# Optimization experiments

Measured on AMD Instinct MI355X. Metric: run time of the kernel, lower is better.

## Reference

```python
import jax, jax.numpy as jnp
import numpy as np

R = 131072          # total proposals (ROIs)
D = 1024            # input feature dim (ShapeSpec.channels)
NUM_CLASSES = 80    # COCO foreground classes
REID_DIM = 256      # reid_feat_dim
BOX_DIM = 4


def setup_inputs() -> dict:
    key = jax.random.key(0)
    ks = jax.random.split(key, 12)
    x = jax.random.normal(ks[0], (R, D), dtype=jnp.float32)
    # cls_score: Linear(D, num_classes+1), init std=0.01, bias 0
    W_cls = 0.01 * jax.random.normal(ks[1], (NUM_CLASSES + 1, D), dtype=jnp.float32)
    b_cls = jnp.zeros((NUM_CLASSES + 1,), dtype=jnp.float32)
    # bbox_pred: Linear(D, num_classes * 4), init std=0.001, bias 0
    W_bbox = 0.001 * jax.random.normal(ks[2], (NUM_CLASSES * BOX_DIM, D), dtype=jnp.float32)
    b_bbox = jnp.zeros((NUM_CLASSES * BOX_DIM,), dtype=jnp.float32)
    # reid_embed_head: MLP(D, 256, 256, 3) -> Linear(D,256), Linear(256,256), Linear(256,256)
    def lin(k, fan_in, fan_out):
        kw, kb = jax.random.split(k)
        bound = 1.0 / np.sqrt(fan_in)
        W = jax.random.uniform(kw, (fan_out, fan_in), minval=-bound, maxval=bound, dtype=jnp.float32)
        b = jax.random.uniform(kb, (fan_out,), minval=-bound, maxval=bound, dtype=jnp.float32)
        return W, b
    W1, b1 = lin(ks[3], D, REID_DIM)
    W2, b2 = lin(ks[4], REID_DIM, REID_DIM)
    W3, b3 = lin(ks[5], REID_DIM, REID_DIM)
    return {"x": x, "W_cls": W_cls, "b_cls": b_cls, "W_bbox": W_bbox, "b_bbox": b_bbox,
            "W1": W1, "b1": b1, "W2": W2, "b2": b2, "W3": W3, "b3": b3}


def reference(x, W_cls, b_cls, W_bbox, b_bbox, W1, b1, W2, b2, W3, b3):
    # x: [R, D] (already flat; torch forward flattens if dim > 2)
    scores = x @ W_cls.T + b_cls                 # [R, K+1]
    proposal_deltas = x @ W_bbox.T + b_bbox      # [R, K*4]
    # MLP with ReLU on all but last layer
    h = jax.nn.relu(x @ W1.T + b1)               # [R, 256]
    h = jax.nn.relu(h @ W2.T + b2)               # [R, 256]
    embeds = h @ W3.T + b3                       # [R, 256]
    return scores, proposal_deltas, embeds
```

## Files before the change

kernel.cpp:

```cpp
#include <hip/hip_runtime.h>
#include <hip/hip_bf16.h>
#include <stdint.h>

#define R_TOT   131072
#define D_IN    1024
#define N_CLS   81
#define N_BOX   320
#define N_H     256
#define N1_USED 657
#define N1_PAD  768
#define NB_COLS 384

typedef __attribute__((ext_vector_type(8))) short short8;
typedef __attribute__((ext_vector_type(4))) float f32x4;

__device__ __forceinline__ unsigned short f2bf(float f) {
  union { float f; unsigned u; } v; v.f = f;
  unsigned r = v.u + 0x7FFFu + ((v.u >> 16) & 1u);
  return (unsigned short)(r >> 16);
}

__device__ __forceinline__ short8 cvt8(float4 a, float4 b) {
  short8 v;
  v[0] = (short)f2bf(a.x); v[1] = (short)f2bf(a.y);
  v[2] = (short)f2bf(a.z); v[3] = (short)f2bf(a.w);
  v[4] = (short)f2bf(b.x); v[5] = (short)f2bf(b.y);
  v[6] = (short)f2bf(b.z); v[7] = (short)f2bf(b.w);
  return v;
}

__device__ __forceinline__ void async_lds16(void* lds, const void* g) {
  __builtin_amdgcn_global_load_lds(
      (const __attribute__((address_space(1))) unsigned int*)g,
      (__attribute__((address_space(3))) unsigned int*)lds, 16, 0, 0);
}

__global__ void prep_w1(const float* __restrict__ Wc, const float* __restrict__ Wb,
                        const float* __restrict__ W1, unsigned short* __restrict__ Wp)
{
  int idx = blockIdx.x * 256 + threadIdx.x;
  int p   = idx / (N1_PAD * 32);
  int rem = idx % (N1_PAD * 32);
  int n   = rem >> 5;
  int kk  = rem & 31;
  int k   = p * 32 + kk;
  float w = 0.f;
  if (n < N_CLS)               w = Wc[(size_t)n * D_IN + k];
  else if (n < N_CLS + N_BOX)  w = Wb[(size_t)(n - N_CLS) * D_IN + k];
  else if (n < N1_USED)        w = W1[(size_t)(n - (N_CLS + N_BOX)) * D_IN + k];
  Wp[idx] = f2bf(w);
}

__global__ void prep_w23(const float* __restrict__ W2, const float* __restrict__ W3,
                         unsigned short* __restrict__ W2b, unsigned short* __restrict__ W3b)
{
  int idx = blockIdx.x * 256 + threadIdx.x;
  if (idx < 65536) W2b[idx] = f2bf(W2[idx]);
  else             W3b[idx - 65536] = f2bf(W3[idx - 65536]);
}

__global__ __launch_bounds__(512) void g1_kernel(
    const float* __restrict__ x, const unsigned short* __restrict__ Wp,
    const float* __restrict__ b_cls, const float* __restrict__ b_box,
    const float* __restrict__ b1,
    float* __restrict__ scores, float* __restrict__ deltas,
    unsigned short* __restrict__ h1)
{
  __shared__ __attribute__((aligned(16))) unsigned short As[64 * 256];

  const int tid  = threadIdx.x;
  const int wave = tid >> 6;
  const int lane = tid & 63;
  const int orig  = blockIdx.x;
  const int work  = (orig & 7) * 512 + (orig >> 3);
  const int m0    = (work >> 1) * 64;
  const int nbase = (work & 1) * NB_COLS;

  const int lr  = lane & 15;
  const int hig = lane >> 4;
  const int g2  = hig * 8;

  f32x4 acc[4][3];
#pragma unroll
  for (int i = 0; i < 4; ++i)
#pragma unroll
    for (int j = 0; j < 3; ++j)
      acc[i][j] = (f32x4){0.f, 0.f, 0.f, 0.f};

  const unsigned short* bptr = Wp + (size_t)(nbase + wave * 48 + lr) * 32 + g2;
  const size_t BSTEP = (size_t)N1_PAD * 32;

  short8 bCur0 = *(const short8*)(bptr);
  short8 bCur1 = *(const short8*)(bptr + 512);
  short8 bCur2 = *(const short8*)(bptr + 1024);
  bptr += BSTEP;

#pragma unroll 2
  for (int kp = 0; kp < 32; ++kp) {
    const int kk = kp & 7;

    if (kk == 0) {
      if (kp > 0) __syncthreads();
      const int c0 = (kp >> 3) * 256;
#pragma unroll
      for (int i = 0; i < 4; ++i) {
        int idx = tid + i * 512;
        int row = idx >> 5, s = idx & 31;
        const float* src = x + (size_t)(m0 + row) * D_IN + c0 + s * 8;
        float4 f0 = *(const float4*)src;
        float4 f1 = *(const float4*)(src + 4);
        *(short8*)&As[row * 256 + ((s ^ (row & 7)) << 3)] = cvt8(f0, f1);
      }
      __syncthreads();
    }

    short8 bn0, bn1, bn2;
    if (kp < 31) {
      bn0 = *(const short8*)(bptr);
      bn1 = *(const short8*)(bptr + 512);
      bn2 = *(const short8*)(bptr + 1024);
      bptr += BSTEP;
    }

    const int sb = kk * 4 + hig;
    __builtin_amdgcn_s_setprio(1);
#pragma unroll
    for (int mi = 0; mi < 4; ++mi) {
      const int r  = mi * 16 + lr;
      const int sl = sb ^ (r & 7);
      short8 af = *(const short8*)&As[r * 256 + (sl << 3)];
      acc[mi][0] = __builtin_amdgcn_mfma_f32_16x16x32_bf16(af, bCur0, acc[mi][0], 0, 0, 0);
      acc[mi][1] = __builtin_amdgcn_mfma_f32_16x16x32_bf16(af, bCur1, acc[mi][1], 0, 0, 0);
      acc[mi][2] = __builtin_amdgcn_mfma_f32_16x16x32_bf16(af, bCur2, acc[mi][2], 0, 0, 0);
    }
    __builtin_amdgcn_s_setprio(0);

    if (kp < 31) { bCur0 = bn0; bCur1 = bn1; bCur2 = bn2; }
  }

  const int rbase = m0 + (hig << 2);
#pragma unroll
  for (int mi = 0; mi < 4; ++mi) {
#pragma unroll
    for (int ni = 0; ni < 3; ++ni) {
      int n = nbase + wave * 48 + ni * 16 + lr;
      if (n >= N1_USED) continue;
      if (n < N_CLS) {
        float bb = b_cls[n];
#pragma unroll
        for (int j = 0; j < 4; ++j) {
          int r = rbase + mi * 16 + j;
          scores[(size_t)r * N_CLS + n] = acc[mi][ni][j] + bb;
        }
      } else if (n < N_CLS + N_BOX) {
        int nb = n - N_CLS;
        float bb = b_box[nb];
#pragma unroll
        for (int j = 0; j < 4; ++j) {
          int r = rbase + mi * 16 + j;
          deltas[(size_t)r * N_BOX + nb] = acc[mi][ni][j] + bb;
        }
      } else {
        int nh = n - (N_CLS + N_BOX);
        float bb = b1[nh];
#pragma unroll
        for (int j = 0; j < 4; ++j) {
          int r = rbase + mi * 16 + j;
          float h = acc[mi][ni][j] + bb;
          h1[(size_t)r * N_H + nh] = f2bf(fmaxf(h, 0.f));
        }
      }
    }
  }
}

__device__ __forceinline__ void g23_stage(unsigned short* Asb, unsigned short* Bsb,
    const unsigned short* __restrict__ A, const unsigned short* __restrict__ Bw,
    int m0, int kp, int tid)
{
  {
    int row = tid >> 2, kq = tid & 3;
    async_lds16((char*)Asb + tid * 16,
                (const char*)(A + (size_t)(m0 + row) * N_H + (size_t)kp * 32 + kq * 8));
  }
#pragma unroll
  for (int i = 0; i < 2; ++i) {
    int chunk = tid + i * 512;
    int row = chunk >> 2, kq = chunk & 3;
    async_lds16((char*)Bsb + chunk * 16,
                (const char*)(Bw + (size_t)row * N_H + (size_t)kp * 32 + kq * 8));
  }
}

template <int RELU, int OUT_BF16>
__global__ __launch_bounds__(512, 1) void g23_kernel(
    const unsigned short* __restrict__ A, const unsigned short* __restrict__ Bw,
    const float* __restrict__ bias, void* __restrict__ outv)
{
  __shared__ __attribute__((aligned(16))) unsigned short As[2][128 * 32];
  __shared__ __attribute__((aligned(16))) unsigned short Bs[2][256 * 32];
  const int tid  = threadIdx.x;
  const int wave = tid >> 6, lane = tid & 63;
  const int wm = wave >> 2, wn = wave & 3;
  const int m0 = blockIdx.x * 128;

  f32x4 acc[4][4];
#pragma unroll
  for (int i = 0; i < 4; ++i)
#pragma unroll
    for (int j = 0; j < 4; ++j)
      acc[i][j] = (f32x4){0.f, 0.f, 0.f, 0.f};

  g23_stage(&As[0][0], &Bs[0][0], A, Bw, m0, 0, tid);
  __syncthreads();

  const int lr = lane & 15;
  const int lk = (lane >> 4) * 8;

  for (int kp = 0; kp < 8; ++kp) {
    const int cur = kp & 1, nxt = cur ^ 1;
    if (kp < 7) g23_stage(&As[nxt][0], &Bs[nxt][0], A, Bw, m0, kp + 1, tid);

    short8 af[4], bfr[4];
#pragma unroll
    for (int mi = 0; mi < 4; ++mi)
      af[mi] = *(const short8*)&As[cur][(wm * 64 + mi * 16 + lr) * 32 + lk];
#pragma unroll
    for (int ni = 0; ni < 4; ++ni)
      bfr[ni] = *(const short8*)&Bs[cur][(wn * 64 + ni * 16 + lr) * 32 + lk];
#pragma unroll
    for (int mi = 0; mi < 4; ++mi)
#pragma unroll
      for (int ni = 0; ni < 4; ++ni)
        acc[mi][ni] = __builtin_amdgcn_mfma_f32_16x16x32_bf16(af[mi], bfr[ni], acc[mi][ni], 0, 0, 0);
    __syncthreads();
  }

#pragma unroll
  for (int mi = 0; mi < 4; ++mi) {
#pragma unroll
    for (int ni = 0; ni < 4; ++ni) {
      int n = wn * 64 + ni * 16 + lr;
      float bb = bias[n];
#pragma unroll
      for (int j = 0; j < 4; ++j) {
        int r = m0 + wm * 64 + mi * 16 + ((lane >> 4) << 2) + j;
        float v = acc[mi][ni][j] + bb;
        if (RELU) v = fmaxf(v, 0.f);
        if (OUT_BF16) ((unsigned short*)outv)[(size_t)r * N_H + n] = f2bf(v);
        else          ((float*)outv)[(size_t)r * N_H + n] = v;
      }
    }
  }
}

extern "C" void kernel_launch(void* const* d_in, const int* in_sizes, int n_in,
                              void* d_out, int out_size, void* d_ws, size_t ws_size,
                              hipStream_t stream)
{
  const float* x     = (const float*)d_in[0];
  const float* W_cls = (const float*)d_in[1];
  const float* b_cls = (const float*)d_in[2];
  const float* W_box = (const float*)d_in[3];
  const float* b_box = (const float*)d_in[4];
  const float* W1    = (const float*)d_in[5];
  const float* b1    = (const float*)d_in[6];
  const float* W2    = (const float*)d_in[7];
  const float* b2    = (const float*)d_in[8];
  const float* W3    = (const float*)d_in[9];
  const float* b3    = (const float*)d_in[10];

  float* scores = (float*)d_out;
  float* deltas = scores + (size_t)R_TOT * N_CLS;
  float* embeds = deltas + (size_t)R_TOT * N_BOX;

  char* ws = (char*)d_ws;
  unsigned short* Wp  = (unsigned short*)ws;
  unsigned short* W2b = (unsigned short*)(ws + 1572864);
  unsigned short* W3b = (unsigned short*)(ws + 1572864 + 131072);
  unsigned short* h   = (unsigned short*)(ws + 1835008);

  hipLaunchKernelGGL(prep_w1, dim3(3072), dim3(256), 0, stream, W_cls, W_box, W1, Wp);
  hipLaunchKernelGGL(prep_w23, dim3(512), dim3(256), 0, stream, W2, W3, W2b, W3b);
  hipLaunchKernelGGL(g1_kernel, dim3(4096), dim3(512), 0, stream,
                     x, Wp, b_cls, b_box, b1, scores, deltas, h);
  hipLaunchKernelGGL((g23_kernel<1, 1>), dim3(R_TOT / 128), dim3(512), 0, stream,
                     h, W2b, b2, (void*)h);
  hipLaunchKernelGGL((g23_kernel<0, 0>), dim3(R_TOT / 128), dim3(512), 0, stream,
                     h, W3b, b3, (void*)embeds);
}
```

Measured before the change: 428.3 us.

## Fuse second and third MLP GEMMs, keeping intermediate activations in LDS

Merges the two reid MLP GEMM kernels into one. The ReLU'd second-layer output for each 128-row tile is written as bf16 into a 64KB XOR-swizzled shared-memory buffer, and the third GEMM reads its A operand from there. This removes one launch and the global write and read of the 128Kx256 bf16 intermediate. In exchange the block uses much more LDS (about 112KB), and the third GEMM streams only W3 through the double buffer.

Measured after the change: 417.1 us, median of 5. -2.6%, faster.

```diff
diff --git a/kernel.cpp b/kernel.cpp
--- a/kernel.cpp
+++ b/kernel.cpp
@@ -174,15 +174,16 @@
   }
 }
 
-__device__ __forceinline__ void g23_stage(unsigned short* Asb, unsigned short* Bsb,
-    const unsigned short* __restrict__ A, const unsigned short* __restrict__ Bw,
-    int m0, int kp, int tid)
-{
-  {
-    int row = tid >> 2, kq = tid & 3;
-    async_lds16((char*)Asb + tid * 16,
-                (const char*)(A + (size_t)(m0 + row) * N_H + (size_t)kp * 32 + kq * 8));
-  }
+__device__ __forceinline__ void gf_stageA(unsigned short* Asb,
+    const unsigned short* __restrict__ A, int m0, int kp, int tid)
+{
+  int row = tid >> 2, kq = tid & 3;
+  async_lds16((char*)Asb + tid * 16,
+              (const char*)(A + (size_t)(m0 + row) * N_H + (size_t)kp * 32 + kq * 8));
+}
+__device__ __forceinline__ void gf_stageB(unsigned short* Bsb,
+    const unsigned short* __restrict__ Bw, int kp, int tid)
+{
 #pragma unroll
   for (int i = 0; i < 2; ++i) {
     int chunk = tid + i * 512;
@@ -192,17 +193,22 @@
   }
 }
 
-template <int RELU, int OUT_BF16>
-__global__ __launch_bounds__(512, 1) void g23_kernel(
-    const unsigned short* __restrict__ A, const unsigned short* __restrict__ Bw,
-    const float* __restrict__ bias, void* __restrict__ outv)
+__global__ __launch_bounds__(512, 1) void g23_fused(
+    const unsigned short* __restrict__ h1, const unsigned short* __restrict__ W2b,
+    const unsigned short* __restrict__ W3b, const float* __restrict__ b2,
+    const float* __restrict__ b3, float* __restrict__ embeds)
 {
   __shared__ __attribute__((aligned(16))) unsigned short As[2][128 * 32];
   __shared__ __attribute__((aligned(16))) unsigned short Bs[2][256 * 32];
+  __shared__ __attribute__((aligned(16))) unsigned short H2[128 * 256];
+
   const int tid  = threadIdx.x;
   const int wave = tid >> 6, lane = tid & 63;
   const int wm = wave >> 2, wn = wave & 3;
   const int m0 = blockIdx.x * 128;
+  const int lr = lane & 15;
+  const int hig = lane >> 4;
+  const int lk = hig * 8;
 
   f32x4 acc[4][4];
 #pragma unroll
@@ -211,15 +217,14 @@
     for (int j = 0; j < 4; ++j)
       acc[i][j] = (f32x4){0.f, 0.f, 0.f, 0.f};
 
-  g23_stage(&As[0][0], &Bs[0][0], A, Bw, m0, 0, tid);
+  gf_stageA(&As[0][0], h1, m0, 0, tid);
+  gf_stageB(&Bs[0][0], W2b, 0, tid);
   __syncthreads();
-
-  const int lr = lane & 15;
-  const int lk = (lane >> 4) * 8;
 
   for (int kp = 0; kp < 8; ++kp) {
     const int cur = kp & 1, nxt = cur ^ 1;
-    if (kp < 7) g23_stage(&As[nxt][0], &Bs[nxt][0], A, Bw, m0, kp + 1, tid);
+    if (kp < 7) { gf_stageA(&As[nxt][0], h1, m0, kp + 1, tid);
+                  gf_stageB(&Bs[nxt][0], W2b, kp + 1, tid); }
 
     short8 af[4], bfr[4];
 #pragma unroll
@@ -241,14 +246,53 @@
 #pragma unroll
     for (int ni = 0; ni < 4; ++ni) {
       int n = wn * 64 + ni * 16 + lr;
-      float bb = bias[n];
+      float bb = b2[n];
 #pragma unroll
       for (int j = 0; j < 4; ++j) {
-        int r = m0 + wm * 64 + mi * 16 + ((lane >> 4) << 2) + j;
-        float v = acc[mi][ni][j] + bb;
-        if (RELU) v = fmaxf(v, 0.f);
-        if (OUT_BF16) ((unsigned short*)outv)[(size_t)r * N_H + n] = f2bf(v);
-        else          ((float*)outv)[(size_t)r * N_H + n] = v;
+        int r = wm * 64 + mi * 16 + (hig << 2) + j;
+        float v = fmaxf(acc[mi][ni][j] + bb, 0.f);
+        H2[r * 256 + (((n >> 3) ^ (r & 7)) << 3) + (n & 7)] = f2bf(v);
+      }
+      acc[mi][ni] = (f32x4){0.f, 0.f, 0.f, 0.f};
+    }
+  }
+  __syncthreads();
+
+  gf_stageB(&Bs[0][0], W3b, 0, tid);
+  __syncthreads();
+
+  for (int kp = 0; kp < 8; ++kp) {
+    const int cur = kp & 1, nxt = cur ^ 1;
+    if (kp < 7) gf_stageB(&Bs[nxt][0], W3b, kp + 1, tid);
+
+    short8 af[4], bfr[4];
+#pragma unroll
+    for (int mi = 0; mi < 4; ++mi) {
+      const int r  = wm * 64 + mi * 16 + lr;
+      const int co = kp * 4 + hig;
+      af[mi] = *(const short8*)&H2[r * 256 + ((co ^ (r & 7)) << 3)];
+    }
+#pragma unroll
+    for (int ni = 0; ni < 4; ++ni)
+      bfr[ni] = *(const short8*)&Bs[cur][(wn * 64 + ni * 16 + lr) * 32 + lk];
+#pragma unroll
+    for (int mi = 0; mi < 4; ++mi)
+#pragma unroll
+      for (int ni = 0; ni < 4; ++ni)
+        acc[mi][ni] = __builtin_amdgcn_mfma_f32_16x16x32_bf16(af[mi], bfr[ni], acc[mi][ni], 0, 0, 0);
+    __syncthreads();
+  }
+
+#pragma unroll
+  for (int mi = 0; mi < 4; ++mi) {
+#pragma unroll
+    for (int ni = 0; ni < 4; ++ni) {
+      int n = wn * 64 + ni * 16 + lr;
+      float bb = b3[n];
+#pragma unroll
+      for (int j = 0; j < 4; ++j) {
+        int r = m0 + wm * 64 + mi * 16 + (hig << 2) + j;
+        embeds[(size_t)r * N_H + n] = acc[mi][ni][j] + bb;
       }
     }
   }
@@ -278,14 +322,12 @@
   unsigned short* Wp  = (unsigned short*)ws;
   unsigned short* W2b = (unsigned short*)(ws + 1572864);
   unsigned short* W3b = (unsigned short*)(ws + 1572864 + 131072);
-  unsigned short* h   = (unsigned short*)(ws + 1835008);
+  unsigned short* h1  = (unsigned short*)(ws + 1835008);
 
   hipLaunchKernelGGL(prep_w1, dim3(3072), dim3(256), 0, stream, W_cls, W_box, W1, Wp);
   hipLaunchKernelGGL(prep_w23, dim3(512), dim3(256), 0, stream, W2, W3, W2b, W3b);
   hipLaunchKernelGGL(g1_kernel, dim3(4096), dim3(512), 0, stream,
-                     x, Wp, b_cls, b_box, b1, scores, deltas, h);
-  hipLaunchKernelGGL((g23_kernel<1, 1>), dim3(R_TOT / 128), dim3(512), 0, stream,
-                     h, W2b, b2, (void*)h);
-  hipLaunchKernelGGL((g23_kernel<0, 0>), dim3(R_TOT / 128), dim3(512), 0, stream,
-                     h, W3b, b3, (void*)embeds);
-}
+                     x, Wp, b_cls, b_box, b1, scores, deltas, h1);
+  hipLaunchKernelGGL(g23_fused, dim3(R_TOT / 128), dim3(512), 0, stream,
+                     h1, W2b, W3b, b2, b3, embeds);
+}
```
